# Performance work log

Measured on AMD Instinct MI355X. Metric: run time of the kernel, lower is better.

Reference implementation:

```python
import jax, jax.numpy as jnp
import numpy as np

B, H, W, C = 4, 64, 64, 256
D = C // 8  # reduction_ratio = 8


def setup_inputs() -> dict:
    key = jax.random.key(0)
    ks = jax.random.split(key, 6)
    scale = 1.0 / np.sqrt(C)
    return {
        "x": jax.random.normal(ks[0], (B, H, W, C), dtype=jnp.float32),
        "Wf": jax.random.normal(ks[1], (C, D), dtype=jnp.float32) * scale,
        "Wg": jax.random.normal(ks[2], (C, D), dtype=jnp.float32) * scale,
        "Wh": jax.random.normal(ks[3], (C, D), dtype=jnp.float32) * scale,
        "Wv": jax.random.normal(ks[4], (D, C), dtype=jnp.float32) * (1.0 / np.sqrt(D)),
        "gamma": jax.random.normal(ks[5], (), dtype=jnp.float32),
    }


def reference(x, Wf, Wg, Wh, Wv, gamma):
    b, h, w, c = x.shape
    n = h * w
    xf = x.reshape(b, n, c)
    # 1x1 convs (no bias) == per-pixel matmuls over channels
    q = xf @ Wf  # [b, n, d]
    k = xf @ Wg  # [b, n, d]
    v = xf @ Wh  # [b, n, d]
    # beta[i, j] = k_i . q_j ; softmax over last (query) axis, unscaled
    beta = jax.nn.softmax(jnp.einsum('bnd,bmd->bnm', k, q), axis=-1)  # [b, n, n]
    o = jnp.einsum('bnm,bmd->bnd', beta, v)  # [b, n, d]
    o = o.reshape(b, h, w, -1) @ Wv  # output 1x1 conv -> [b, h, w, c]
    return gamma * o + x
```

## Files before the change

kernel.cpp:

```cpp
#include <hip/hip_runtime.h>
#include <hip/hip_bf16.h>
#include <stdint.h>


typedef __attribute__((ext_vector_type(8))) short bf16x8;
typedef __attribute__((ext_vector_type(4))) float f32x4;
typedef unsigned short ushort_t;

static __device__ __forceinline__ ushort_t f2bf(float f) {
    __hip_bfloat16 h = __float2bfloat16(f);
    return __builtin_bit_cast(ushort_t, h);
}
static __device__ __forceinline__ float bf2f(ushort_t u) {
    return __bfloat162float(__builtin_bit_cast(__hip_bfloat16, u));
}
static __device__ __forceinline__ ushort_t f2bf_fast(float f) {
    unsigned u = __builtin_bit_cast(unsigned, f);
    return (ushort_t)((u + 0x8000u) >> 16);
}

#define NROWS 16384
#define NTOK  4096
#define QKS   40
#define PVS   72
#define OPART (NROWS * 32)
#define LOG2E 1.44269504088896f

__global__ __launch_bounds__(256) void qkv_kernel(
    const float* __restrict__ x,
    const float* __restrict__ Wf, const float* __restrict__ Wg,
    const float* __restrict__ Wh,
    ushort_t* __restrict__ qh,
    ushort_t* __restrict__ kh, ushort_t* __restrict__ kl,
    ushort_t* __restrict__ vT)
{
    __shared__ __align__(16) ushort_t xh[32 * QKS];
    __shared__ __align__(16) ushort_t xl[32 * QKS];

    const int tid  = threadIdx.x;
    const int wave = tid >> 6;
    const int lane = tid & 63;
    const int ln15 = lane & 15;
    const int quad = lane >> 4;
    const int row0 = blockIdx.x * 32;
    const int rg     = wave & 1;
    const int cgbase = wave >> 1;
    const int r  = tid >> 3;
    const int pp = (tid & 7) * 4;

    f32x4 acc[3];
    #pragma unroll
    for (int ci = 0; ci < 3; ++ci) acc[ci] = (f32x4){0.f, 0.f, 0.f, 0.f};

    float4 xa = *reinterpret_cast<const float4*>(&x[(row0 + r) * 256 + pp]);

    for (int k0 = 0; k0 < 256; k0 += 32) {
        bf16x8 bh[3], bl[3];
        #pragma unroll
        for (int ci = 0; ci < 3; ++ci) {
            int cg = cgbase + ci * 2;
            const float* Wsrc = (cg < 2) ? Wf : (cg < 4) ? Wg : Wh;
            int c = (cg & 1) * 16 + ln15;
            ushort_t hv8[8], lv8[8];
            #pragma unroll
            for (int j = 0; j < 8; ++j) {
                float w = Wsrc[(k0 + quad * 8 + j) * 32 + c];
                ushort_t hi = f2bf(w);
                hv8[j] = hi;
                lv8[j] = f2bf(w - bf2f(hi));
            }
            bh[ci] = *reinterpret_cast<bf16x8*>(hv8);
            bl[ci] = *reinterpret_cast<bf16x8*>(lv8);
        }
        float fv[4];
        *reinterpret_cast<float4*>(fv) = xa;
        ushort_t hv[4], lv[4];
        #pragma unroll
        for (int j = 0; j < 4; ++j) {
            hv[j] = f2bf(fv[j]);
            lv[j] = f2bf(fv[j] - bf2f(hv[j]));
        }
        __syncthreads();
        *reinterpret_cast<uint2*>(&xh[r * QKS + pp]) = *reinterpret_cast<uint2*>(hv);
        *reinterpret_cast<uint2*>(&xl[r * QKS + pp]) = *reinterpret_cast<uint2*>(lv);
        __syncthreads();
        if (k0 < 224)
            xa = *reinterpret_cast<const float4*>(&x[(row0 + r) * 256 + k0 + 32 + pp]);

        const bf16x8 ah = *reinterpret_cast<const bf16x8*>(
            &xh[(rg * 16 + ln15) * QKS + quad * 8]);
        const bf16x8 al = *reinterpret_cast<const bf16x8*>(
            &xl[(rg * 16 + ln15) * QKS + quad * 8]);
        #pragma unroll
        for (int ci = 0; ci < 3; ++ci) {
            acc[ci] = __builtin_amdgcn_mfma_f32_16x16x32_bf16(ah, bh[ci], acc[ci], 0, 0, 0);
            acc[ci] = __builtin_amdgcn_mfma_f32_16x16x32_bf16(al, bh[ci], acc[ci], 0, 0, 0);
            acc[ci] = __builtin_amdgcn_mfma_f32_16x16x32_bf16(ah, bl[ci], acc[ci], 0, 0, 0);
        }
    }

    #pragma unroll
    for (int ci = 0; ci < 3; ++ci) {
        int cg = cgbase + ci * 2;
        int cc = (cg & 1) * 16 + ln15;
        int rowb = row0 + rg * 16 + quad * 4;
        if (cg < 2) {
            #pragma unroll
            for (int rr = 0; rr < 4; ++rr)
                qh[(rowb + rr) * 32 + cc] = f2bf(acc[ci][rr]);
        } else if (cg < 4) {
            #pragma unroll
            for (int rr = 0; rr < 4; ++rr) {
                float val = acc[ci][rr] * LOG2E;
                ushort_t hi = f2bf(val);
                kh[(rowb + rr) * 32 + cc] = hi;
                kl[(rowb + rr) * 32 + cc] = f2bf(val - bf2f(hi));
            }
        } else {
            int bb = row0 >> 12;
            int m  = (row0 & 4095) + rg * 16 + quad * 4;
            ushort4 h4;
            h4.x = f2bf(acc[ci][0]);
            h4.y = f2bf(acc[ci][1]);
            h4.z = f2bf(acc[ci][2]);
            h4.w = f2bf(acc[ci][3]);
            *reinterpret_cast<ushort4*>(&vT[bb * 131072 + cc * 4096 + m]) = h4;
        }
    }
}

__global__ __launch_bounds__(256, 4) void attn_kernel(
    const ushort_t* __restrict__ qhg,
    const ushort_t* __restrict__ khg, const ushort_t* __restrict__ klg,
    const ushort_t* __restrict__ vT,
    float* __restrict__ o_part, float* __restrict__ l_part)
{
    __shared__ __align__(16) ushort_t Khs[64 * QKS];
    __shared__ __align__(16) ushort_t Kls[64 * QKS];
    __shared__ __align__(16) ushort_t Qhs[2][64 * QKS];
    __shared__ __align__(16) ushort_t Vth[2][32 * PVS];
    __shared__ __align__(16) ushort_t Ps[4 * 16 * PVS];

    const int tid  = threadIdx.x;
    const int wave = tid >> 6;
    const int lane = tid & 63;
    const int ln15 = lane & 15;
    const int quad = lane >> 4;

    const int rowtile = blockIdx.x & 255;
    const int chunk   = blockIdx.x >> 8;
    const int b    = rowtile >> 6;
    const int n0   = (rowtile & 63) * 64;
    const int base = b * NTOK;
    const int bb   = b * 131072;
    const int mt0  = chunk * 16;

    const int r  = tid >> 2;
    const int p  = (tid & 3) * 8;
    const int vd = tid >> 3;
    const int vm = (tid & 7) * 8;

    {
        uint4 a0 = *reinterpret_cast<const uint4*>(&khg[(base + n0 + r) * 32 + p]);
        *reinterpret_cast<uint4*>(&Khs[r * QKS + p]) = a0;
        uint4 a1 = *reinterpret_cast<const uint4*>(&klg[(base + n0 + r) * 32 + p]);
        *reinterpret_cast<uint4*>(&Kls[r * QKS + p]) = a1;
        int m0 = mt0 * 64;
        uint4 t0 = *reinterpret_cast<const uint4*>(&qhg[(base + m0 + r) * 32 + p]);
        *reinterpret_cast<uint4*>(&Qhs[0][r * QKS + p]) = t0;
        uint4 v0 = *reinterpret_cast<const uint4*>(&vT[bb + vd * 4096 + m0 + vm]);
        *reinterpret_cast<uint4*>(&Vth[0][vd * PVS + vm]) = v0;
    }
    __syncthreads();

    const bf16x8 khf = *reinterpret_cast<const bf16x8*>(
        &Khs[(wave * 16 + ln15) * QKS + quad * 8]);
    const bf16x8 klf = *reinterpret_cast<const bf16x8*>(
        &Kls[(wave * 16 + ln15) * QKS + quad * 8]);

    f32x4 accO[2];
    accO[0] = (f32x4){0.f, 0.f, 0.f, 0.f};
    accO[1] = (f32x4){0.f, 0.f, 0.f, 0.f};
    float lacc[4] = {0.f, 0.f, 0.f, 0.f};

    int buf = 0;
    for (int it = 0; it < 16; ++it) {
        uint4 nqh, nvh;
        if (it < 15) {
            int m1 = (mt0 + it + 1) * 64;
            nqh = *reinterpret_cast<const uint4*>(&qhg[(base + m1 + r) * 32 + p]);
            nvh = *reinterpret_cast<const uint4*>(&vT[bb + vd * 4096 + m1 + vm]);
        }

        f32x4 st[4];
        #pragma unroll
        for (int t = 0; t < 4; ++t) {
            const bf16x8 qf = *reinterpret_cast<const bf16x8*>(
                &Qhs[buf][(t * 16 + ln15) * QKS + quad * 8]);
            f32x4 s = __builtin_amdgcn_mfma_f32_16x16x32_bf16(
                khf, qf, (f32x4){0.f, 0.f, 0.f, 0.f}, 0, 0, 0);
            s = __builtin_amdgcn_mfma_f32_16x16x32_bf16(klf, qf, s, 0, 0, 0);
            st[t] = s;
        }

        #pragma unroll
        for (int t = 0; t < 4; ++t)
            #pragma unroll
            for (int rr = 0; rr < 4; ++rr)
                st[t][rr] = exp2f(st[t][rr]);
        #pragma unroll
        for (int rr = 0; rr < 4; ++rr)
            lacc[rr] += st[0][rr] + st[1][rr] + st[2][rr] + st[3][rr];

        ushort_t* pw = &Ps[wave * 16 * PVS];
        #pragma unroll
        for (int t = 0; t < 4; ++t)
            #pragma unroll
            for (int rr = 0; rr < 4; ++rr)
                pw[(quad * 4 + rr) * PVS + ((t ^ quad) & 3) * 16 + ln15] =
                    f2bf_fast(st[t][rr]);

        const int rq = (ln15 >> 2) & 3;
        #pragma unroll
        for (int kc = 0; kc < 2; ++kc) {
            const bf16x8 af = *reinterpret_cast<const bf16x8*>(
                &pw[ln15 * PVS + (((kc * 32 + quad * 8) ^ (rq * 16)))]);
            #pragma unroll
            for (int s01 = 0; s01 < 2; ++s01) {
                const bf16x8 bhf = *reinterpret_cast<const bf16x8*>(
                    &Vth[buf][(s01 * 16 + ln15) * PVS + kc * 32 + quad * 8]);
                accO[s01] = __builtin_amdgcn_mfma_f32_16x16x32_bf16(af, bhf, accO[s01], 0, 0, 0);
            }
        }

        if (it < 15) {
            *reinterpret_cast<uint4*>(&Qhs[buf ^ 1][r * QKS + p]) = nqh;
            *reinterpret_cast<uint4*>(&Vth[buf ^ 1][vd * PVS + vm]) = nvh;
            __syncthreads();
        }
        buf ^= 1;
    }

    #pragma unroll
    for (int rr = 0; rr < 4; ++rr) {
        float s0 = lacc[rr];
        #pragma unroll
        for (int off = 1; off < 16; off <<= 1)
            s0 += __shfl_xor(s0, off);
        lacc[rr] = s0;
    }
    const int row_base = base + n0 + wave * 16 + quad * 4;
    float* op = o_part + (size_t)chunk * OPART;
    if (ln15 == 0) {
        #pragma unroll
        for (int rr = 0; rr < 4; ++rr)
            l_part[chunk * NROWS + row_base + rr] = lacc[rr];
    }
    #pragma unroll
    for (int s01 = 0; s01 < 2; ++s01)
        #pragma unroll
        for (int rr = 0; rr < 4; ++rr)
            op[(row_base + rr) * 32 + s01 * 16 + ln15] = accO[s01][rr];
}

__global__ __launch_bounds__(256) void out_kernel(
    const float* __restrict__ o_part, const float* __restrict__ l_part,
    const float* __restrict__ Wv, const float* __restrict__ x,
    const float* __restrict__ gamma, float* __restrict__ out)
{
    __shared__ float wv[8192];
    __shared__ float orow[32][32];
    __shared__ float linv[32];
    const int tid  = threadIdx.x;
    const int row0 = blockIdx.x * 32;

    for (int i = tid; i < 8192; i += 256) wv[i] = Wv[i];
    for (int i = tid; i < 1024; i += 256) {
        int rr = i >> 5, d = i & 31;
        int idx = (row0 + rr) * 32 + d;
        orow[rr][d] = o_part[idx] + o_part[OPART + idx]
                    + o_part[2 * OPART + idx] + o_part[3 * OPART + idx];
    }
    if (tid < 32) {
        int row = row0 + tid;
        linv[tid] = 1.0f / (l_part[row] + l_part[NROWS + row]
                          + l_part[2 * NROWS + row] + l_part[3 * NROWS + row]);
    }
    __syncthreads();

    const float g = gamma[0];
    #pragma unroll 4
    for (int rc = 0; rc < 32; rc += 8) {
        float acc[8];
        #pragma unroll
        for (int rr = 0; rr < 8; ++rr) acc[rr] = 0.f;
        for (int d = 0; d < 32; ++d) {
            float wvd = wv[d * 256 + tid];
            #pragma unroll
            for (int rr = 0; rr < 8; ++rr) acc[rr] += orow[rc + rr][d] * wvd;
        }
        #pragma unroll
        for (int rr = 0; rr < 8; ++rr) {
            int row = row0 + rc + rr;
            out[row * 256 + tid] = g * acc[rr] * linv[rc + rr] + x[row * 256 + tid];
        }
    }
}

extern "C" void kernel_launch(void* const* d_in, const int* in_sizes, int n_in,
                              void* d_out, int out_size, void* d_ws, size_t ws_size,
                              hipStream_t stream)
{
    const float* x     = (const float*)d_in[0];
    const float* Wf    = (const float*)d_in[1];
    const float* Wg    = (const float*)d_in[2];
    const float* Wh    = (const float*)d_in[3];
    const float* Wv    = (const float*)d_in[4];
    const float* gamma = (const float*)d_in[5];
    float* out = (float*)d_out;

    ushort_t* qh = (ushort_t*)d_ws;
    ushort_t* kh = qh + NROWS * 32;
    ushort_t* kl = kh + NROWS * 32;
    ushort_t* vT = kl + NROWS * 32;
    float* o_part = (float*)(vT + NROWS * 32);
    float* l_part = o_part + (size_t)4 * OPART;

    qkv_kernel<<<dim3(512), dim3(256), 0, stream>>>(x, Wf, Wg, Wh, qh, kh, kl, vT);
    attn_kernel<<<dim3(1024), dim3(256), 0, stream>>>(qh, kh, kl, vT, o_part, l_part);
    out_kernel<<<dim3(512), dim3(256), 0, stream>>>(o_part, l_part, Wv, x, gamma, out);
}
```

Baseline: 128.3 us.

## Read Q/V fragments directly from global memory and split keys into 8 chunks

The attention kernel stops staging Q and V tiles through double-buffered shared memory and loads MFMA fragments straight from global/L2, which removes the per-iteration __syncthreads. The key dimension is split into 8 chunks instead of 4, doubling the grid to raise parallelism. The output kernel now sums 8 partials. The cost is redundant global loads across the four waves, which each read the same Q and V tiles, plus twice the partial-sum traffic.

Result: slower. 147.6 us (+15.0%).

```diff
diff --git a/kernel.cpp b/kernel.cpp
--- a/kernel.cpp
+++ b/kernel.cpp
@@ -24,6 +24,7 @@
 #define QKS   40
 #define PVS   72
 #define OPART (NROWS * 32)
+#define NCHUNK 8
 #define LOG2E 1.44269504088896f
 
 __global__ __launch_bounds__(256) void qkv_kernel(
@@ -129,16 +130,12 @@
     }
 }
 
-__global__ __launch_bounds__(256, 4) void attn_kernel(
+__global__ __launch_bounds__(256) void attn_kernel(
     const ushort_t* __restrict__ qhg,
     const ushort_t* __restrict__ khg, const ushort_t* __restrict__ klg,
     const ushort_t* __restrict__ vT,
     float* __restrict__ o_part, float* __restrict__ l_part)
 {
-    __shared__ __align__(16) ushort_t Khs[64 * QKS];
-    __shared__ __align__(16) ushort_t Kls[64 * QKS];
-    __shared__ __align__(16) ushort_t Qhs[2][64 * QKS];
-    __shared__ __align__(16) ushort_t Vth[2][32 * PVS];
     __shared__ __align__(16) ushort_t Ps[4 * 16 * PVS];
 
     const int tid  = threadIdx.x;
@@ -153,50 +150,29 @@
     const int n0   = (rowtile & 63) * 64;
     const int base = b * NTOK;
     const int bb   = b * 131072;
-    const int mt0  = chunk * 16;
-
-    const int r  = tid >> 2;
-    const int p  = (tid & 3) * 8;
-    const int vd = tid >> 3;
-    const int vm = (tid & 7) * 8;
-
-    {
-        uint4 a0 = *reinterpret_cast<const uint4*>(&khg[(base + n0 + r) * 32 + p]);
-        *reinterpret_cast<uint4*>(&Khs[r * QKS + p]) = a0;
-        uint4 a1 = *reinterpret_cast<const uint4*>(&klg[(base + n0 + r) * 32 + p]);
-        *reinterpret_cast<uint4*>(&Kls[r * QKS + p]) = a1;
-        int m0 = mt0 * 64;
-        uint4 t0 = *reinterpret_cast<const uint4*>(&qhg[(base + m0 + r) * 32 + p]);
-        *reinterpret_cast<uint4*>(&Qhs[0][r * QKS + p]) = t0;
-        uint4 v0 = *reinterpret_cast<const uint4*>(&vT[bb + vd * 4096 + m0 + vm]);
-        *reinterpret_cast<uint4*>(&Vth[0][vd * PVS + vm]) = v0;
-    }
-    __syncthreads();
+    const int m0   = chunk * 512;
 
     const bf16x8 khf = *reinterpret_cast<const bf16x8*>(
-        &Khs[(wave * 16 + ln15) * QKS + quad * 8]);
+        &khg[(base + n0 + wave * 16 + ln15) * 32 + quad * 8]);
     const bf16x8 klf = *reinterpret_cast<const bf16x8*>(
-        &Kls[(wave * 16 + ln15) * QKS + quad * 8]);
+        &klg[(base + n0 + wave * 16 + ln15) * 32 + quad * 8]);
 
     f32x4 accO[2];
     accO[0] = (f32x4){0.f, 0.f, 0.f, 0.f};
     accO[1] = (f32x4){0.f, 0.f, 0.f, 0.f};
     float lacc[4] = {0.f, 0.f, 0.f, 0.f};
 
-    int buf = 0;
-    for (int it = 0; it < 16; ++it) {
-        uint4 nqh, nvh;
-        if (it < 15) {
-            int m1 = (mt0 + it + 1) * 64;
-            nqh = *reinterpret_cast<const uint4*>(&qhg[(base + m1 + r) * 32 + p]);
-            nvh = *reinterpret_cast<const uint4*>(&vT[bb + vd * 4096 + m1 + vm]);
-        }
+    ushort_t* pw = &Ps[wave * 16 * PVS];
+    const int rq = (ln15 >> 2) & 3;
+
+    for (int it = 0; it < 8; ++it) {
+        const int mt = m0 + it * 64;
 
         f32x4 st[4];
         #pragma unroll
         for (int t = 0; t < 4; ++t) {
             const bf16x8 qf = *reinterpret_cast<const bf16x8*>(
-                &Qhs[buf][(t * 16 + ln15) * QKS + quad * 8]);
+                &qhg[(base + mt + t * 16 + ln15) * 32 + quad * 8]);
             f32x4 s = __builtin_amdgcn_mfma_f32_16x16x32_bf16(
                 khf, qf, (f32x4){0.f, 0.f, 0.f, 0.f}, 0, 0, 0);
             s = __builtin_amdgcn_mfma_f32_16x16x32_bf16(klf, qf, s, 0, 0, 0);
@@ -212,7 +188,6 @@
         for (int rr = 0; rr < 4; ++rr)
             lacc[rr] += st[0][rr] + st[1][rr] + st[2][rr] + st[3][rr];
 
-        ushort_t* pw = &Ps[wave * 16 * PVS];
         #pragma unroll
         for (int t = 0; t < 4; ++t)
             #pragma unroll
@@ -220,7 +195,6 @@
                 pw[(quad * 4 + rr) * PVS + ((t ^ quad) & 3) * 16 + ln15] =
                     f2bf_fast(st[t][rr]);
 
-        const int rq = (ln15 >> 2) & 3;
         #pragma unroll
         for (int kc = 0; kc < 2; ++kc) {
             const bf16x8 af = *reinterpret_cast<const bf16x8*>(
@@ -228,17 +202,11 @@
             #pragma unroll
             for (int s01 = 0; s01 < 2; ++s01) {
                 const bf16x8 bhf = *reinterpret_cast<const bf16x8*>(
-                    &Vth[buf][(s01 * 16 + ln15) * PVS + kc * 32 + quad * 8]);
-                accO[s01] = __builtin_amdgcn_mfma_f32_16x16x32_bf16(af, bhf, accO[s01], 0, 0, 0);
+                    &vT[bb + (s01 * 16 + ln15) * 4096 + mt + kc * 32 + quad * 8]);
+                accO[s01] = __builtin_amdgcn_mfma_f32_16x16x32_bf16(
+                    af, bhf, accO[s01], 0, 0, 0);
             }
         }
-
-        if (it < 15) {
-            *reinterpret_cast<uint4*>(&Qhs[buf ^ 1][r * QKS + p]) = nqh;
-            *reinterpret_cast<uint4*>(&Vth[buf ^ 1][vd * PVS + vm]) = nvh;
-            __syncthreads();
-        }
-        buf ^= 1;
     }
 
     #pragma unroll
@@ -278,13 +246,17 @@
     for (int i = tid; i < 1024; i += 256) {
         int rr = i >> 5, d = i & 31;
         int idx = (row0 + rr) * 32 + d;
-        orow[rr][d] = o_part[idx] + o_part[OPART + idx]
-                    + o_part[2 * OPART + idx] + o_part[3 * OPART + idx];
+        float s = 0.f;
+        #pragma unroll
+        for (int c = 0; c < NCHUNK; ++c) s += o_part[(size_t)c * OPART + idx];
+        orow[rr][d] = s;
     }
     if (tid < 32) {
         int row = row0 + tid;
-        linv[tid] = 1.0f / (l_part[row] + l_part[NROWS + row]
-                          + l_part[2 * NROWS + row] + l_part[3 * NROWS + row]);
+        float s = 0.f;
+        #pragma unroll
+        for (int c = 0; c < NCHUNK; ++c) s += l_part[c * NROWS + row];
+        linv[tid] = 1.0f / s;
     }
     __syncthreads();
 
@@ -324,9 +296,9 @@
     ushort_t* kl = kh + NROWS * 32;
     ushort_t* vT = kl + NROWS * 32;
     float* o_part = (float*)(vT + NROWS * 32);
-    float* l_part = o_part + (size_t)4 * OPART;
+    float* l_part = o_part + (size_t)NCHUNK * OPART;
 
     qkv_kernel<<<dim3(512), dim3(256), 0, stream>>>(x, Wf, Wg, Wh, qh, kh, kl, vT);
-    attn_kernel<<<dim3(1024), dim3(256), 0, stream>>>(qh, kh, kl, vT, o_part, l_part);
+    attn_kernel<<<dim3(256 * NCHUNK), dim3(256), 0, stream>>>(qh, kh, kl, vT, o_part, l_part);
     out_kernel<<<dim3(512), dim3(256), 0, stream>>>(o_part, l_part, Wv, x, gamma, out);
 }
```
